# Kernel tuning notes

Hardware: AMD Instinct MI355X
Metric: run time of the kernel (lower is better)

Reference implementation:

```python
import jax, jax.numpy as jnp
import numpy as np

HID = 128; H = 8; D = HID // H; L = 2; IN = 128; OUT = 32
ND = 20000; NF = 50000; E = 400000
SQRT_D = float(np.sqrt(D))
LN_EPS = 1e-5


def setup_inputs() -> dict:
    key = jax.random.key(0)
    ks = jax.random.split(key, 16)
    s = 1.0 / np.sqrt(HID)
    n = lambda k, sh, sc=1.0: jax.random.normal(k, sh, jnp.float32) * sc
    return dict(
        x_device=n(ks[0], (ND, IN)),
        x_feature=n(ks[1], (NF, IN)),
        e_df_src=jax.random.randint(ks[2], (E,), 0, ND),
        e_df_dst=jax.random.randint(ks[3], (E,), 0, NF),
        e_fd_src=jax.random.randint(ks[4], (E,), 0, NF),
        e_fd_dst=jax.random.randint(ks[5], (E,), 0, ND),
        W_dev_in=n(ks[6], (IN, HID), s), b_dev_in=jnp.zeros((HID,), jnp.float32),
        W_feat_in=n(ks[7], (IN, HID), s), b_feat_in=jnp.zeros((HID,), jnp.float32),
        Wk=n(ks[8], (L, 2, HID, HID), s), bk=jnp.zeros((L, 2, HID), jnp.float32),
        Wq=n(ks[9], (L, 2, HID, HID), s), bq=jnp.zeros((L, 2, HID), jnp.float32),
        Wv=n(ks[10], (L, 2, HID, HID), s), bv=jnp.zeros((L, 2, HID), jnp.float32),
        a_rel=n(ks[11], (L, 2, H, D, D), 1.0 / np.sqrt(D)),
        m_rel=n(ks[12], (L, 2, H, D, D), 1.0 / np.sqrt(D)),
        p_rel=jnp.ones((L, 2, H), jnp.float32),
        Wa=n(ks[13], (L, 2, HID, HID), s), ba=jnp.zeros((L, 2, HID), jnp.float32),
        skip=jnp.ones((L, 2), jnp.float32),
        ln_g=jnp.ones((L, 2, HID), jnp.float32), ln_b=jnp.zeros((L, 2, HID), jnp.float32),
        W_out=n(ks[14], (HID, OUT), s), b_out=jnp.zeros((OUT,), jnp.float32),
    )


def _layer_norm(x, g, b):
    m = x.mean(-1, keepdims=True)
    v = ((x - m) ** 2).mean(-1, keepdims=True)
    return (x - m) * jax.lax.rsqrt(v + LN_EPS) * g + b


def _edge_agg(q_dst, k_src, v_src, a_r, m_r, p_r, src, dst, n_dst):
    # per-edge-type relation transforms of source k/v: [N_src,H,D]
    kt = jnp.einsum('nhd,hde->nhe', k_src, a_r)
    vt = jnp.einsum('nhd,hde->nhe', v_src, m_r)
    # per-edge attention logits [E,H], scaled by relation prior
    logit = (q_dst[dst] * kt[src]).sum(-1) * p_r / SQRT_D
    # segment softmax over incoming edges of each dst node (per edge type)
    mx = jax.ops.segment_max(logit, dst, num_segments=n_dst)
    ex = jnp.exp(logit - mx[dst])
    sm = jax.ops.segment_sum(ex, dst, num_segments=n_dst)
    alpha = ex / (sm[dst] + 1e-16)
    # attention-weighted message scatter-sum -> [n_dst,H,D]
    return jax.ops.segment_sum(vt[src] * alpha[..., None], dst, num_segments=n_dst)


def _forward(x_device, x_feature, W_dev_in, b_dev_in, W_feat_in, b_feat_in,
             Wk, bk, Wq, bq, Wv, bv, a_rel, m_rel, p_rel, Wa, ba, skip,
             ln_g, ln_b, W_out, b_out, e_df_src, e_df_dst, e_fd_src, e_fd_dst):
    x_d = jax.nn.relu(x_device @ W_dev_in + b_dev_in)
    x_f = jax.nn.relu(x_feature @ W_feat_in + b_feat_in)
    for l in range(L):
        xs = (x_d, x_f)  # node-type 0 = device, 1 = feature
        k = [(xs[t] @ Wk[l, t] + bk[l, t]).reshape(-1, H, D) for t in range(2)]
        q = [(xs[t] @ Wq[l, t] + bq[l, t]).reshape(-1, H, D) for t in range(2)]
        v = [(xs[t] @ Wv[l, t] + bv[l, t]).reshape(-1, H, D) for t in range(2)]
        # edge type 0: device -> feature ; edge type 1: feature -> device
        agg_f = _edge_agg(q[1], k[0], v[0], a_rel[l, 0], m_rel[l, 0], p_rel[l, 0],
                          e_df_src, e_df_dst, NF)
        agg_d = _edge_agg(q[0], k[1], v[1], a_rel[l, 1], m_rel[l, 1], p_rel[l, 1],
                          e_fd_src, e_fd_dst, ND)
        new = []
        for t, agg in ((0, agg_d), (1, agg_f)):
            o = jax.nn.gelu(agg.reshape(-1, HID), approximate=False) @ Wa[l, t] + ba[l, t]
            sk = jax.nn.sigmoid(skip[l, t])
            o = sk * o + (1.0 - sk) * xs[t]              # HGTConv skip
            new.append(_layer_norm(xs[t] + o, ln_g[l, t], ln_b[l, t]))  # wrapper residual+LN (dropout=identity in eval)
        x_d, x_f = new
    return x_d @ W_out + b_out


def reference(x_device, x_feature, e_df_src, e_df_dst, e_fd_src, e_fd_dst,
              W_dev_in, b_dev_in, W_feat_in, b_feat_in, Wk, bk, Wq, bq, Wv, bv,
              a_rel, m_rel, p_rel, Wa, ba, skip, ln_g, ln_b, W_out, b_out):
    return _forward(x_device, x_feature, W_dev_in, b_dev_in, W_feat_in, b_feat_in,
                    Wk, bk, Wq, bq, Wv, bv, a_rel, m_rel, p_rel, Wa, ba, skip,
                    ln_g, ln_b, W_out, b_out, e_df_src, e_df_dst, e_fd_src, e_fd_dst)
```

## Files before the change

kernel.cpp:

```cpp
#include <hip/hip_runtime.h>
#include <math.h>

#define ND 20000
#define NF 50000
#define NE 400000
#define NT (NF + ND)
#define NBKT 256
#define BKTW 274

typedef __attribute__((ext_vector_type(8))) short short8;
typedef __attribute__((ext_vector_type(4))) float f32x4;
typedef unsigned short us;

static __device__ __forceinline__ us f2bf(float f) {
    unsigned u = __builtin_bit_cast(unsigned, f);
    u += 0x7FFF + ((u >> 16) & 1);
    return (us)(u >> 16);
}
static __device__ __forceinline__ float bf2f(us h) {
    return __builtin_bit_cast(float, (unsigned)h << 16);
}
static __device__ __forceinline__ float bflo(unsigned u) {
    return __builtin_bit_cast(float, u << 16);
}
static __device__ __forceinline__ float bfhi(unsigned u) {
    return __builtin_bit_cast(float, u & 0xFFFF0000u);
}
static __device__ __forceinline__ float gelu_f(float x) {
    return 0.5f * x * (1.0f + erff(x * 0.70710678118654752f));
}

__global__ void k_hist_prep(const int* __restrict__ dA, const int* __restrict__ dB,
                            int* __restrict__ blockhist, int HB,
                            const float* __restrict__ W_dev_in, const float* __restrict__ W_feat_in,
                            const float* __restrict__ Wq, const float* __restrict__ Wk,
                            const float* __restrict__ Wv, const float* __restrict__ Wa,
                            const float* __restrict__ b_dev_in, const float* __restrict__ b_feat_in,
                            const float* __restrict__ bq, const float* __restrict__ bk,
                            const float* __restrict__ bv, const float* __restrict__ ba,
                            const float* __restrict__ a_rel, const float* __restrict__ m_rel,
                            const float* __restrict__ p_rel,
                            us* __restrict__ WT, float* __restrict__ B_all) {
    __shared__ int hist[NBKT];
    if ((int)blockIdx.x < HB) {
        hist[threadIdx.x] = 0;
        __syncthreads();
        int base_e = blockIdx.x * 4096;
        #pragma unroll
        for (int j = 0; j < 16; ++j) {
            int e = base_e + j * 256 + threadIdx.x;
            if (e < 2 * NE) {
                int g = (e < NE) ? dA[e] : (NF + dB[e - NE]);
                atomicAdd(&hist[g / BKTW], 1);
            }
        }
        __syncthreads();
        blockhist[blockIdx.x * NBKT + threadIdx.x] = hist[threadIdx.x];
        return;
    }
    int idx = (blockIdx.x - HB) * 256 + threadIdx.x;
    if (idx < 18 * 16384) {
        int k = idx & 127, c = (idx >> 7) & 127, id = idx >> 14;
        float val;
        if (id == 0) val = W_dev_in[k * 128 + c];
        else if (id == 1) val = W_feat_in[k * 128 + c];
        else if (id < 6) val = Wq[(id - 2) * 16384 + k * 128 + c];
        else if (id < 10) {
            int lt = id - 6, h = c >> 4, e = c & 15;
            const float* A = a_rel + (lt * 8 + h) * 256;
            const float* Ws = Wk + lt * 16384 + k * 128 + h * 16;
            float sm = 0.f;
            #pragma unroll
            for (int d = 0; d < 16; ++d) sm += Ws[d] * A[d * 16 + e];
            val = sm * p_rel[lt * 8 + h] * 0.25f;
        } else if (id < 14) {
            int lt = id - 10, h = c >> 4, e = c & 15;
            const float* A = m_rel + (lt * 8 + h) * 256;
            const float* Ws = Wv + lt * 16384 + k * 128 + h * 16;
            float sm = 0.f;
            #pragma unroll
            for (int d = 0; d < 16; ++d) sm += Ws[d] * A[d * 16 + e];
            val = sm;
        } else val = Wa[(id - 14) * 16384 + k * 128 + c];
        WT[(size_t)id * 16384 + (((c * 128 + k)) ^ ((c & 7) << 3))] = f2bf(val);
    } else {
        int j = idx - 18 * 16384;
        if (j >= 18 * 128) return;
        int c = j & 127, id = j >> 7;
        float v;
        if (id == 0) v = b_dev_in[c];
        else if (id == 1) v = b_feat_in[c];
        else if (id < 6) v = bq[(id - 2) * 128 + c];
        else if (id < 10) {
            int lt = id - 6, h = c >> 4, e = c & 15;
            const float* A = a_rel + (lt * 8 + h) * 256;
            const float* bs = bk + lt * 128 + h * 16;
            float sm = 0.f;
            #pragma unroll
            for (int d = 0; d < 16; ++d) sm += bs[d] * A[d * 16 + e];
            v = sm * p_rel[lt * 8 + h] * 0.25f;
        } else if (id < 14) {
            int lt = id - 10, h = c >> 4, e = c & 15;
            const float* A = m_rel + (lt * 8 + h) * 256;
            const float* bs = bv + lt * 128 + h * 16;
            float sm = 0.f;
            #pragma unroll
            for (int d = 0; d < 16; ++d) sm += bs[d] * A[d * 16 + e];
            v = sm;
        } else v = ba[(id - 14) * 128 + c];
        B_all[j] = v;
    }
}

__global__ void k_scanA(int* __restrict__ blockhist, int* __restrict__ totals, int HB) {
    __shared__ int sd[256];
    int b = blockIdx.x, t = threadIdx.x;
    int v = (t < HB) ? blockhist[t * NBKT + b] : 0;
    sd[t] = v; __syncthreads();
    for (int off = 1; off < 256; off <<= 1) {
        int add = (t >= off) ? sd[t - off] : 0;
        __syncthreads();
        sd[t] += add;
        __syncthreads();
    }
    if (t < HB) blockhist[t * NBKT + b] = sd[t] - v;
    if (t == 255) totals[b] = sd[255];
}

__global__ void k_scanB(const int* __restrict__ totals, int* __restrict__ base) {
    __shared__ int sd[256];
    int t = threadIdx.x;
    int v = totals[t];
    sd[t] = v; __syncthreads();
    for (int off = 1; off < 256; off <<= 1) {
        int add = (t >= off) ? sd[t - off] : 0;
        __syncthreads();
        sd[t] += add;
        __syncthreads();
    }
    base[t] = sd[t] - v;
    if (t == 255) base[256] = sd[255];
}

__global__ void k_scatter(const int* __restrict__ sA, const int* __restrict__ dA,
                          const int* __restrict__ sB, const int* __restrict__ dB,
                          const int* __restrict__ blockhist, const int* __restrict__ base,
                          uint2* __restrict__ pairs) {
    __shared__ int lcur[NBKT];
    int t = threadIdx.x;
    lcur[t] = base[t] + blockhist[blockIdx.x * NBKT + t];
    __syncthreads();
    int base_e = blockIdx.x * 4096;
    #pragma unroll
    for (int j = 0; j < 16; ++j) {
        int e = base_e + j * 256 + t;
        if (e < 2 * NE) {
            int src, g;
            if (e < NE) { src = sA[e]; g = dA[e]; }
            else        { src = sB[e - NE]; g = NF + dB[e - NE]; }
            int pos = atomicAdd(&lcur[g / BKTW], 1);
            pairs[pos] = make_uint2((unsigned)src, (unsigned)g);
        }
    }
}

__global__ void k_bucket_csr(const uint2* __restrict__ pairs, const int* __restrict__ base,
                             int* __restrict__ rs, int* __restrict__ esrc) {
    __shared__ int cnt[BKTW];
    __shared__ int excl[BKTW];
    int b = blockIdx.x, t = threadIdx.x;
    int start = base[b], end = base[b + 1];
    int g0 = b * BKTW;
    for (int i = t; i < BKTW; i += 256) cnt[i] = 0;
    __syncthreads();
    for (int i = start + t; i < end; i += 256)
        atomicAdd(&cnt[(int)pairs[i].y - g0], 1);
    __syncthreads();
    if (t < 64) {
        int lane = t;
        int vals[5]; int s = 0;
        #pragma unroll
        for (int j = 0; j < 5; ++j) {
            int i = lane * 5 + j;
            vals[j] = (i < BKTW) ? cnt[i] : 0;
            s += vals[j];
        }
        int incl = s;
        #pragma unroll
        for (int off = 1; off < 64; off <<= 1) {
            int n = __shfl_up(incl, off);
            if (lane >= off) incl += n;
        }
        int run = incl - s;
        #pragma unroll
        for (int j = 0; j < 5; ++j) {
            int i = lane * 5 + j;
            if (i < BKTW) excl[i] = run;
            run += vals[j];
        }
    }
    __syncthreads();
    int nloc = min(BKTW, NT - g0);
    for (int i = t; i < nloc; i += 256) rs[g0 + i] = start + excl[i];
    if (b == NBKT - 1 && t == 0) rs[NT] = base[NBKT];
    __syncthreads();
    for (int i = start + t; i < end; i += 256) {
        uint2 p = pairs[i];
        int pos = start + atomicAdd(&excl[(int)p.y - g0], 1);
        esrc[pos] = (int)p.x;
    }
}

template<int MODE, int AF32, int RELU>
__global__ __launch_bounds__(256) void mfma_gemm2(
    const void* __restrict__ X0, const void* __restrict__ X1,
    const us* __restrict__ WT0, const float* __restrict__ Ball,
    us* __restrict__ Y0, us* __restrict__ Y1,
    int N0, int N1, int GB0, int widbase,
    us* __restrict__ K0, us* __restrict__ K1,
    const float* __restrict__ skipv, const float* __restrict__ lng,
    const float* __restrict__ lnb) {
    __shared__ us Wlds[16384];
    const int type = (blockIdx.x >= (unsigned)GB0) ? 1 : 0;
    const int bx = blockIdx.x - (type ? GB0 : 0);
    const int N = type ? N1 : N0;
    const void* Xv = type ? X1 : X0;
    const int NP = (MODE == 1) ? 3 : 1;

    const int lane = threadIdx.x & 63;
    const int wave = threadIdx.x >> 6;
    const int row_base = bx * 128 + wave * 32;
    const int l15 = lane & 15, lg = lane >> 4;
    const int kbase = lg * 8;

    const char* gsrc0 = (const char*)(WT0 + (size_t)(widbase + type) * 16384)
                        + wave * 8192 + lane * 16;
    {
        char* ldst = (char*)Wlds + wave * 8192;
        #pragma unroll
        for (int i = 0; i < 8; ++i) {
            __builtin_amdgcn_global_load_lds(
                (const __attribute__((address_space(1))) void*)(gsrc0 + i * 1024),
                (__attribute__((address_space(3))) void*)(ldst + i * 1024),
                16, 0, 0);
        }
    }

    short8 a[2][4];
    #pragma unroll
    for (int mf = 0; mf < 2; ++mf) {
        int r = row_base + mf * 16 + l15;
        r = r < N ? r : N - 1;
        if (AF32) {
            const float* Xf = (const float*)Xv + (size_t)r * 128;
            #pragma unroll
            for (int kf = 0; kf < 4; ++kf) {
                float4 lo = *(const float4*)(Xf + kf * 32 + kbase);
                float4 hi = *(const float4*)(Xf + kf * 32 + kbase + 4);
                short8 t;
                t[0] = (short)f2bf(lo.x); t[1] = (short)f2bf(lo.y);
                t[2] = (short)f2bf(lo.z); t[3] = (short)f2bf(lo.w);
                t[4] = (short)f2bf(hi.x); t[5] = (short)f2bf(hi.y);
                t[6] = (short)f2bf(hi.z); t[7] = (short)f2bf(hi.w);
                a[mf][kf] = t;
            }
        } else {
            const us* Xb = (const us*)Xv + (size_t)r * 128;
            #pragma unroll
            for (int kf = 0; kf < 4; ++kf)
                a[mf][kf] = *(const short8*)(Xb + kf * 32 + kbase);
        }
    }

    __syncthreads();

    const unsigned swz = (unsigned)((l15 & 7) << 4);

    for (int p = 0; p < NP; ++p) {
        const int wid = widbase + type + 4 * p;
        const float* bias = Ball + wid * 128;

        f32x4 acc[2][8];
        #pragma unroll
        for (int mf = 0; mf < 2; ++mf)
            #pragma unroll
            for (int cf = 0; cf < 8; ++cf) acc[mf][cf] = (f32x4){0.f, 0.f, 0.f, 0.f};

        #pragma unroll
        for (int cf = 0; cf < 8; ++cf) {
            const unsigned rowbyte = (unsigned)((cf * 16 + l15) * 256 + kbase * 2);
            #pragma unroll
            for (int kf = 0; kf < 4; ++kf) {
                short8 b = *(const short8*)((const char*)Wlds + ((rowbyte + kf * 64) ^ swz));
                acc[0][cf] = __builtin_amdgcn_mfma_f32_16x16x32_bf16(a[0][kf], b, acc[0][cf], 0, 0, 0);
                acc[1][cf] = __builtin_amdgcn_mfma_f32_16x16x32_bf16(a[1][kf], b, acc[1][cf], 0, 0, 0);
            }
        }

        if (MODE == 1 && p + 1 < NP) {
            __syncthreads();
            const char* gsrc = (const char*)(WT0 + (size_t)(widbase + type + 4 * (p + 1)) * 16384)
                               + wave * 8192 + lane * 16;
            char* ldst = (char*)Wlds + wave * 8192;
            #pragma unroll
            for (int i = 0; i < 8; ++i) {
                __builtin_amdgcn_global_load_lds(
                    (const __attribute__((address_space(1))) void*)(gsrc + i * 1024),
                    (__attribute__((address_space(3))) void*)(ldst + i * 1024),
                    16, 0, 0);
            }
        }

        float bval[8];
        #pragma unroll
        for (int cf = 0; cf < 8; ++cf) bval[cf] = bias[cf * 16 + l15];

        if (MODE == 2) {
            const int lt = widbase - 14 + type;
            float sk = 1.f / (1.f + __expf(-skipv[lt]));
            float gv[8], bv2[8];
            #pragma unroll
            for (int cf = 0; cf < 8; ++cf) {
                gv[cf]  = lng[(size_t)lt * 128 + cf * 16 + l15];
                bv2[cf] = lnb[(size_t)lt * 128 + cf * 16 + l15];
            }
            us* xw = type ? K1 : K0;
            #pragma unroll
            for (int mf = 0; mf < 2; ++mf)
                #pragma unroll
                for (int r = 0; r < 4; ++r) {
                    int grow = row_base + mf * 16 + lg * 4 + r;
                    if (grow >= N) continue;
                    float t[8];
                    float sum = 0.f;
                    #pragma unroll
                    for (int cf = 0; cf < 8; ++cf) {
                        float o = acc[mf][cf][r] + bval[cf];
                        float x = bf2f(xw[(size_t)grow * 128 + cf * 16 + l15]);
                        t[cf] = (2.f - sk) * x + sk * o;
                        sum += t[cf];
                    }
                    sum += __shfl_xor(sum, 1); sum += __shfl_xor(sum, 2);
                    sum += __shfl_xor(sum, 4); sum += __shfl_xor(sum, 8);
                    float mean = sum * (1.0f / 128.0f);
                    float vs = 0.f;
                    #pragma unroll
                    for (int cf = 0; cf < 8; ++cf) { t[cf] -= mean; vs += t[cf] * t[cf]; }
                    vs += __shfl_xor(vs, 1); vs += __shfl_xor(vs, 2);
                    vs += __shfl_xor(vs, 4); vs += __shfl_xor(vs, 8);
                    float inv = rsqrtf(vs * (1.0f / 128.0f) + 1e-5f);
                    #pragma unroll
                    for (int cf = 0; cf < 8; ++cf)
                        xw[(size_t)grow * 128 + cf * 16 + l15] = f2bf(t[cf] * inv * gv[cf] + bv2[cf]);
                }
        } else {
            #pragma unroll
            for (int mf = 0; mf < 2; ++mf)
                #pragma unroll
                for (int r = 0; r < 4; ++r) {
                    int grow = row_base + mf * 16 + lg * 4 + r;
                    if (grow >= N) continue;
                    #pragma unroll
                    for (int cf = 0; cf < 8; ++cf) {
                        float v = acc[mf][cf][r] + bval[cf];
                        if (RELU) v = fmaxf(v, 0.f);
                        us val = f2bf(v);
                        int col = cf * 16 + l15;
                        if (MODE == 0 || p == 0) {
                            (type ? Y1 : Y0)[(size_t)grow * 128 + col] = val;
                        } else {
                            (type ? K1 : K0)[(size_t)grow * 256 + (p - 1) * 128 + col] = val;
                        }
                    }
                }
        }

        if (MODE == 1 && p + 1 < NP) __syncthreads();
    }
}

__global__ __launch_bounds__(256) void gemm_out_k(
    const us* __restrict__ X, const float* __restrict__ W,
    const float* __restrict__ bias, float* __restrict__ Y, int N) {
    __shared__ float Ws[128 * 32];
    __shared__ float Xs[8][128];
    const int tid = threadIdx.x;
    const int row0 = blockIdx.x * 8;
    #pragma unroll
    for (int it = 0; it < 16; ++it) Ws[it * 256 + tid] = W[it * 256 + tid];
    #pragma unroll
    for (int it = 0; it < 2; ++it) {
        int idx = it * 256 + tid;
        int rr = idx >> 6, kp = idx & 63;
        int gr = row0 + rr;
        unsigned u = (gr < N) ? *(const unsigned*)(X + (size_t)gr * 128 + kp * 2) : 0u;
        Xs[rr][kp * 2]     = bflo(u);
        Xs[rr][kp * 2 + 1] = bfhi(u);
    }
    __syncthreads();
    const int rr = tid >> 5, c = tid & 31;
    float acc = bias[c];
    #pragma unroll 8
    for (int k = 0; k < 128; ++k)
        acc = fmaf(Xs[rr][k], Ws[k * 32 + c], acc);
    int gr = row0 + rr;
    if (gr < N) Y[(size_t)gr * 32 + c] = acc;
}

#define EDGE_STEP(kc, vc, pidx)                                        \
    {                                                                  \
        float part = qv[0] * bflo(kc.x);                               \
        part = fmaf(qv[1], bfhi(kc.x), part);                          \
        part = fmaf(qv[2], bflo(kc.y), part);                          \
        part = fmaf(qv[3], bfhi(kc.y), part);                          \
        part = fmaf(qv[4], bflo(kc.z), part);                          \
        part = fmaf(qv[5], bfhi(kc.z), part);                          \
        part = fmaf(qv[6], bflo(kc.w), part);                          \
        part = fmaf(qv[7], bfhi(kc.w), part);                          \
        part += __shfl_xor(part, 1);                                   \
        float w = ((pidx) < p1) ? __expf(part) : 0.f;                  \
        s += w;                                                        \
        a[0] = fmaf(w, bflo(vc.x), a[0]);                              \
        a[1] = fmaf(w, bfhi(vc.x), a[1]);                              \
        a[2] = fmaf(w, bflo(vc.y), a[2]);                              \
        a[3] = fmaf(w, bfhi(vc.y), a[3]);                              \
        a[4] = fmaf(w, bflo(vc.z), a[4]);                              \
        a[5] = fmaf(w, bfhi(vc.z), a[5]);                              \
        a[6] = fmaf(w, bflo(vc.w), a[6]);                              \
        a[7] = fmaf(w, bfhi(vc.w), a[7]);                              \
    }

__global__ __launch_bounds__(256) void edge_agg5(
    const us* __restrict__ qf, const us* __restrict__ qd,
    const us* __restrict__ kvf, const us* __restrict__ kvd,
    const int* __restrict__ rs, const int* __restrict__ esrc,
    us* __restrict__ aggf, us* __restrict__ aggd) {
    int g = (blockIdx.x * 256 + threadIdx.x) >> 4;
    int li = threadIdx.x & 15;
    if (g >= NT) return;
    const us *q, *kv; us* agg; int dst;
    if (g < NF) { dst = g;      q = qf; kv = kvd; agg = aggf; }
    else        { dst = g - NF; q = qd; kv = kvf; agg = aggd; }

    uint4 qb = *(const uint4*)(q + (size_t)dst * 128 + li * 8);
    float qv[8];
    qv[0] = bflo(qb.x); qv[1] = bfhi(qb.x);
    qv[2] = bflo(qb.y); qv[3] = bfhi(qb.y);
    qv[4] = bflo(qb.z); qv[5] = bfhi(qb.z);
    qv[6] = bflo(qb.w); qv[7] = bfhi(qb.w);

    const int p0 = rs[g], p1 = rs[g + 1];
    float s = 0.f;
    float a[8];
    #pragma unroll
    for (int j = 0; j < 8; ++j) a[j] = 0.f;

    const size_t loff = (size_t)li * 8;
    uint4 kA0, vA0, kA1, vA1, kB0, vB0, kB1, vB1;
    int sN0, sN1, sN2, sN3;

    if (p0 < p1) {
        const int last = p1 - 1;
        int i0 = p0, i1 = min(p0 + 1, last), i2 = min(p0 + 2, last), i3 = min(p0 + 3, last);
        int s0 = esrc[i0], s1 = esrc[i1], s2 = esrc[i2], s3 = esrc[i3];
        kA0 = *(const uint4*)(kv + (size_t)s0 * 256 + loff);
        vA0 = *(const uint4*)(kv + (size_t)s0 * 256 + 128 + loff);
        kA1 = *(const uint4*)(kv + (size_t)s1 * 256 + loff);
        vA1 = *(const uint4*)(kv + (size_t)s1 * 256 + 128 + loff);
        kB0 = *(const uint4*)(kv + (size_t)s2 * 256 + loff);
        vB0 = *(const uint4*)(kv + (size_t)s2 * 256 + 128 + loff);
        kB1 = *(const uint4*)(kv + (size_t)s3 * 256 + loff);
        vB1 = *(const uint4*)(kv + (size_t)s3 * 256 + 128 + loff);
        sN0 = esrc[min(p0 + 4, last)];
        sN1 = esrc[min(p0 + 5, last)];
        sN2 = esrc[min(p0 + 6, last)];
        sN3 = esrc[min(p0 + 7, last)];

        for (int p = p0; p < p1; p += 4) {
            const int lastc = last;
            EDGE_STEP(kA0, vA0, p);
            EDGE_STEP(kA1, vA1, p + 1);
            kA0 = *(const uint4*)(kv + (size_t)sN0 * 256 + loff);
            vA0 = *(const uint4*)(kv + (size_t)sN0 * 256 + 128 + loff);
            kA1 = *(const uint4*)(kv + (size_t)sN1 * 256 + loff);
            vA1 = *(const uint4*)(kv + (size_t)sN1 * 256 + 128 + loff);
            sN0 = esrc[min(p + 8, lastc)];
            sN1 = esrc[min(p + 9, lastc)];
            EDGE_STEP(kB0, vB0, p + 2);
            EDGE_STEP(kB1, vB1, p + 3);
            kB0 = *(const uint4*)(kv + (size_t)sN2 * 256 + loff);
            vB0 = *(const uint4*)(kv + (size_t)sN2 * 256 + 128 + loff);
            kB1 = *(const uint4*)(kv + (size_t)sN3 * 256 + loff);
            vB1 = *(const uint4*)(kv + (size_t)sN3 * 256 + 128 + loff);
            sN2 = esrc[min(p + 10, lastc)];
            sN3 = esrc[min(p + 11, lastc)];
        }
    }

    float r = 1.0f / (s + 1e-16f);
    unsigned o[4];
    #pragma unroll
    for (int j = 0; j < 4; ++j) {
        us lo = f2bf(gelu_f(a[2 * j] * r));
        us hi = f2bf(gelu_f(a[2 * j + 1] * r));
        o[j] = (unsigned)lo | ((unsigned)hi << 16);
    }
    *(uint4*)(agg + (size_t)dst * 128 + li * 8) = make_uint4(o[0], o[1], o[2], o[3]);
}

extern "C" void kernel_launch(void* const* d_in, const int* in_sizes, int n_in,
                              void* d_out, int out_size, void* d_ws, size_t ws_size,
                              hipStream_t stream) {
    const float* x_device = (const float*)d_in[0];
    const float* x_feature = (const float*)d_in[1];
    const int* e_df_src = (const int*)d_in[2];
    const int* e_df_dst = (const int*)d_in[3];
    const int* e_fd_src = (const int*)d_in[4];
    const int* e_fd_dst = (const int*)d_in[5];
    const float* W_dev_in = (const float*)d_in[6];
    const float* b_dev_in = (const float*)d_in[7];
    const float* W_feat_in = (const float*)d_in[8];
    const float* b_feat_in = (const float*)d_in[9];
    const float* Wk = (const float*)d_in[10];
    const float* bk = (const float*)d_in[11];
    const float* Wq = (const float*)d_in[12];
    const float* bq = (const float*)d_in[13];
    const float* Wv = (const float*)d_in[14];
    const float* bv = (const float*)d_in[15];
    const float* a_rel = (const float*)d_in[16];
    const float* m_rel = (const float*)d_in[17];
    const float* p_rel = (const float*)d_in[18];
    const float* Wa = (const float*)d_in[19];
    const float* ba = (const float*)d_in[20];
    const float* skip = (const float*)d_in[21];
    const float* ln_g = (const float*)d_in[22];
    const float* ln_b = (const float*)d_in[23];
    const float* W_out = (const float*)d_in[24];
    const float* b_out = (const float*)d_in[25];

    char* ws = (char*)d_ws;
    size_t off = 0;
    auto alloc = [&](size_t bytes) -> void* {
        void* p = ws + off;
        off = (off + bytes + 255) & ~(size_t)255;
        return p;
    };
    us* xd     = (us*)alloc((size_t)ND * 128 * 2);
    us* xf     = (us*)alloc((size_t)NF * 128 * 2);
    us* q_d    = (us*)alloc((size_t)ND * 128 * 2);
    us* q_f    = (us*)alloc((size_t)NF * 128 * 2);
    us* kv_d   = (us*)alloc((size_t)ND * 256 * 2);
    us* kv_f   = (us*)alloc((size_t)NF * 256 * 2);
    us* agg_d  = (us*)alloc((size_t)ND * 128 * 2);
    us* agg_f  = (us*)alloc((size_t)NF * 128 * 2);
    us* WT     = (us*)alloc((size_t)18 * 16384 * 2);
    float* B_all = (float*)alloc(18 * 128 * 4);
    int* rs     = (int*)alloc((size_t)(NT + 1) * 4);
    int* esrc   = (int*)alloc((size_t)(2 * NE + 8) * 4);
    uint2* pairs = (uint2*)alloc((size_t)2 * NE * 8);
    int* blockhist = (int*)alloc((size_t)200 * NBKT * 4);
    int* totals = (int*)alloc(NBKT * 4);
    int* base   = (int*)alloc((NBKT + 1) * 4);

    const int HB = (2 * NE + 4095) / 4096;
    const int PB = (18 * 16384 + 18 * 128 + 255) / 256;

    k_hist_prep<<<HB + PB, 256, 0, stream>>>(
        e_df_dst, e_fd_dst, blockhist, HB,
        W_dev_in, W_feat_in, Wq, Wk, Wv, Wa,
        b_dev_in, b_feat_in, bq, bk, bv, ba,
        a_rel, m_rel, p_rel, WT, B_all);
    k_scanA<<<NBKT, 256, 0, stream>>>(blockhist, totals, HB);
    k_scanB<<<1, 256, 0, stream>>>(totals, base);
    k_scatter<<<HB, 256, 0, stream>>>(e_df_src, e_df_dst, e_fd_src, e_fd_dst,
                                      blockhist, base, pairs);
    k_bucket_csr<<<NBKT, 256, 0, stream>>>(pairs, base, rs, esrc);

    const int GBD = (ND + 127) / 128, GBF = (NF + 127) / 128;

    mfma_gemm2<0, 1, 1><<<GBD + GBF, 256, 0, stream>>>(
        x_device, x_feature, WT, B_all, xd, xf, ND, NF, GBD, 0,
        nullptr, nullptr, nullptr, nullptr, nullptr);

    for (int l = 0; l < 2; ++l) {
        mfma_gemm2<1, 0, 0><<<GBD + GBF, 256, 0, stream>>>(
            xd, xf, WT, B_all, q_d, q_f, ND, NF, GBD, 2 + l * 2,
            kv_d, kv_f, nullptr, nullptr, nullptr);

        edge_agg5<<<((NT * 16) + 255) / 256, 256, 0, stream>>>(
            q_f, q_d, kv_f, kv_d, rs, esrc, agg_f, agg_d);

        mfma_gemm2<2, 0, 0><<<GBD + GBF, 256, 0, stream>>>(
            agg_d, agg_f, WT, B_all, nullptr, nullptr, ND, NF, GBD, 14 + l * 2,
            xd, xf, skip, ln_g, ln_b);
    }

    gemm_out_k<<<(ND + 7) / 8, 256, 0, stream>>>(xd, W_out, b_out, (float*)d_out, ND);
}
```

Baseline: 267.7 us.

## Store V in FP8 and split K/V buffers; fold bucket scan into consumers

The QKV GEMM now writes K as a separate bf16 array and V as a separate FP8 (e4m3) array, and edge aggregation reads 8 bytes of V per lane instead of 16, decoding with the hardware pk_f32_fp8 conversion. This cuts the gather traffic in the memory-bound edge kernel. Separately, the single-block k_scanB launch is removed and its 256-wide prefix scan is recomputed redundantly inside k_scatter and k_bucket_csr. FP8 values lose precision, which risks tolerance failures, and the redundant scans add a little work per block.

```diff
diff --git a/kernel.cpp b/kernel.cpp
--- a/kernel.cpp
+++ b/kernel.cpp
@@ -10,7 +10,9 @@
 
 typedef __attribute__((ext_vector_type(8))) short short8;
 typedef __attribute__((ext_vector_type(4))) float f32x4;
+typedef __attribute__((ext_vector_type(2))) float f32x2;
 typedef unsigned short us;
+typedef unsigned char u8;
 
 static __device__ __forceinline__ us f2bf(float f) {
     unsigned u = __builtin_bit_cast(unsigned, f);
@@ -28,6 +30,22 @@
 }
 static __device__ __forceinline__ float gelu_f(float x) {
     return 0.5f * x * (1.0f + erff(x * 0.70710678118654752f));
+}
+
+static __device__ __forceinline__ u8 f2fp8(float f) {
+    unsigned u = __builtin_bit_cast(unsigned, f);
+    unsigned s = (u >> 24) & 0x80u;
+    unsigned a = u & 0x7FFFFFFFu;
+    if (a >= 0x43E00000u) return (u8)(s | 0x7Eu);
+    if (a < 0x3C800000u) {
+        float af = __builtin_bit_cast(float, a);
+        unsigned q = (unsigned)(af * 512.0f + 0.5f);
+        return (u8)(s | q);
+    }
+    unsigned r = a + 0x7FFFFu + ((a >> 20) & 1u);
+    unsigned e8 = (r >> 23) - 120u;
+    unsigned m3 = (r >> 20) & 7u;
+    return (u8)(s | (e8 << 3) | m3);
 }
 
 __global__ void k_hist_prep(const int* __restrict__ dA, const int* __restrict__ dB,
@@ -127,28 +145,22 @@
     if (t == 255) totals[b] = sd[255];
 }
 
-__global__ void k_scanB(const int* __restrict__ totals, int* __restrict__ base) {
-    __shared__ int sd[256];
-    int t = threadIdx.x;
-    int v = totals[t];
-    sd[t] = v; __syncthreads();
-    for (int off = 1; off < 256; off <<= 1) {
-        int add = (t >= off) ? sd[t - off] : 0;
-        __syncthreads();
-        sd[t] += add;
-        __syncthreads();
-    }
-    base[t] = sd[t] - v;
-    if (t == 255) base[256] = sd[255];
-}
-
 __global__ void k_scatter(const int* __restrict__ sA, const int* __restrict__ dA,
                           const int* __restrict__ sB, const int* __restrict__ dB,
-                          const int* __restrict__ blockhist, const int* __restrict__ base,
+                          const int* __restrict__ blockhist, const int* __restrict__ totals,
                           uint2* __restrict__ pairs) {
     __shared__ int lcur[NBKT];
+    __shared__ int sdb[NBKT];
     int t = threadIdx.x;
-    lcur[t] = base[t] + blockhist[blockIdx.x * NBKT + t];
+    int tv = totals[t];
+    sdb[t] = tv; __syncthreads();
+    for (int off = 1; off < 256; off <<= 1) {
+        int add = (t >= off) ? sdb[t - off] : 0;
+        __syncthreads();
+        sdb[t] += add;
+        __syncthreads();
+    }
+    lcur[t] = (sdb[t] - tv) + blockhist[blockIdx.x * NBKT + t];
     __syncthreads();
     int base_e = blockIdx.x * 4096;
     #pragma unroll
@@ -164,12 +176,24 @@
     }
 }
 
-__global__ void k_bucket_csr(const uint2* __restrict__ pairs, const int* __restrict__ base,
+__global__ void k_bucket_csr(const uint2* __restrict__ pairs, const int* __restrict__ totals,
                              int* __restrict__ rs, int* __restrict__ esrc) {
     __shared__ int cnt[BKTW];
     __shared__ int excl[BKTW];
+    __shared__ int sdb[NBKT];
+    __shared__ int sde[NBKT];
     int b = blockIdx.x, t = threadIdx.x;
-    int start = base[b], end = base[b + 1];
+    int tv = totals[t];
+    sdb[t] = tv; __syncthreads();
+    for (int off = 1; off < 256; off <<= 1) {
+        int add = (t >= off) ? sdb[t - off] : 0;
+        __syncthreads();
+        sdb[t] += add;
+        __syncthreads();
+    }
+    sde[t] = sdb[t] - tv;
+    __syncthreads();
+    int start = sde[b], end = sdb[b];
     int g0 = b * BKTW;
     for (int i = t; i < BKTW; i += 256) cnt[i] = 0;
     __syncthreads();
@@ -202,7 +226,7 @@
     __syncthreads();
     int nloc = min(BKTW, NT - g0);
     for (int i = t; i < nloc; i += 256) rs[g0 + i] = start + excl[i];
-    if (b == NBKT - 1 && t == 0) rs[NT] = base[NBKT];
+    if (b == NBKT - 1 && t == 0) rs[NT] = sdb[255];
     __syncthreads();
     for (int i = start + t; i < end; i += 256) {
         uint2 p = pairs[i];
@@ -218,6 +242,7 @@
     us* __restrict__ Y0, us* __restrict__ Y1,
     int N0, int N1, int GB0, int widbase,
     us* __restrict__ K0, us* __restrict__ K1,
+    u8* __restrict__ V0, u8* __restrict__ V1,
     const float* __restrict__ skipv, const float* __restrict__ lng,
     const float* __restrict__ lnb) {
     __shared__ us Wlds[16384];
@@ -233,14 +258,14 @@
     const int l15 = lane & 15, lg = lane >> 4;
     const int kbase = lg * 8;
 
-    const char* gsrc0 = (const char*)(WT0 + (size_t)(widbase + type) * 16384)
-                        + wave * 8192 + lane * 16;
     {
+        const char* gsrc = (const char*)(WT0 + (size_t)(widbase + type) * 16384)
+                           + wave * 8192 + lane * 16;
         char* ldst = (char*)Wlds + wave * 8192;
         #pragma unroll
         for (int i = 0; i < 8; ++i) {
             __builtin_amdgcn_global_load_lds(
-                (const __attribute__((address_space(1))) void*)(gsrc0 + i * 1024),
+                (const __attribute__((address_space(1))) void*)(gsrc + i * 1024),
                 (__attribute__((address_space(3))) void*)(ldst + i * 1024),
                 16, 0, 0);
         }
@@ -364,12 +389,13 @@
                     for (int cf = 0; cf < 8; ++cf) {
                         float v = acc[mf][cf][r] + bval[cf];
                         if (RELU) v = fmaxf(v, 0.f);
-                        us val = f2bf(v);
                         int col = cf * 16 + l15;
                         if (MODE == 0 || p == 0) {
-                            (type ? Y1 : Y0)[(size_t)grow * 128 + col] = val;
+                            (type ? Y1 : Y0)[(size_t)grow * 128 + col] = f2bf(v);
+                        } else if (p == 1) {
+                            (type ? K1 : K0)[(size_t)grow * 128 + col] = f2bf(v);
                         } else {
-                            (type ? K1 : K0)[(size_t)grow * 256 + (p - 1) * 128 + col] = val;
+                            (type ? V1 : V0)[(size_t)grow * 128 + col] = f2fp8(v);
                         }
                     }
                 }
@@ -420,27 +446,32 @@
         part += __shfl_xor(part, 1);                                   \
         float w = ((pidx) < p1) ? __expf(part) : 0.f;                  \
         s += w;                                                        \
-        a[0] = fmaf(w, bflo(vc.x), a[0]);                              \
-        a[1] = fmaf(w, bfhi(vc.x), a[1]);                              \
-        a[2] = fmaf(w, bflo(vc.y), a[2]);                              \
-        a[3] = fmaf(w, bfhi(vc.y), a[3]);                              \
-        a[4] = fmaf(w, bflo(vc.z), a[4]);                              \
-        a[5] = fmaf(w, bfhi(vc.z), a[5]);                              \
-        a[6] = fmaf(w, bflo(vc.w), a[6]);                              \
-        a[7] = fmaf(w, bfhi(vc.w), a[7]);                              \
-    }
-
-__global__ __launch_bounds__(256) void edge_agg5(
+        f32x2 v01 = __builtin_amdgcn_cvt_pk_f32_fp8((int)vc.x, false); \
+        f32x2 v23 = __builtin_amdgcn_cvt_pk_f32_fp8((int)vc.x, true);  \
+        f32x2 v45 = __builtin_amdgcn_cvt_pk_f32_fp8((int)vc.y, false); \
+        f32x2 v67 = __builtin_amdgcn_cvt_pk_f32_fp8((int)vc.y, true);  \
+        a[0] = fmaf(w, v01.x, a[0]);                                   \
+        a[1] = fmaf(w, v01.y, a[1]);                                   \
+        a[2] = fmaf(w, v23.x, a[2]);                                   \
+        a[3] = fmaf(w, v23.y, a[3]);                                   \
+        a[4] = fmaf(w, v45.x, a[4]);                                   \
+        a[5] = fmaf(w, v45.y, a[5]);                                   \
+        a[6] = fmaf(w, v67.x, a[6]);                                   \
+        a[7] = fmaf(w, v67.y, a[7]);                                   \
+    }
+
+__global__ __launch_bounds__(256) void edge_agg6(
     const us* __restrict__ qf, const us* __restrict__ qd,
-    const us* __restrict__ kvf, const us* __restrict__ kvd,
+    const us* __restrict__ ktf, const us* __restrict__ ktd,
+    const u8* __restrict__ v8f, const u8* __restrict__ v8d,
     const int* __restrict__ rs, const int* __restrict__ esrc,
     us* __restrict__ aggf, us* __restrict__ aggd) {
     int g = (blockIdx.x * 256 + threadIdx.x) >> 4;
     int li = threadIdx.x & 15;
     if (g >= NT) return;
-    const us *q, *kv; us* agg; int dst;
-    if (g < NF) { dst = g;      q = qf; kv = kvd; agg = aggf; }
-    else        { dst = g - NF; q = qd; kv = kvf; agg = aggd; }
+    const us *q, *kt; const u8* v8; us* agg; int dst;
+    if (g < NF) { dst = g;      q = qf; kt = ktd; v8 = v8d; agg = aggf; }
+    else        { dst = g - NF; q = qd; kt = ktf; v8 = v8f; agg = aggd; }
 
     uint4 qb = *(const uint4*)(q + (size_t)dst * 128 + li * 8);
     float qv[8];
@@ -456,21 +487,22 @@
     for (int j = 0; j < 8; ++j) a[j] = 0.f;
 
     const size_t loff = (size_t)li * 8;
-    uint4 kA0, vA0, kA1, vA1, kB0, vB0, kB1, vB1;
+    uint4 kA0, kA1, kB0, kB1;
+    uint2 vA0, vA1, vB0, vB1;
     int sN0, sN1, sN2, sN3;
 
     if (p0 < p1) {
         const int last = p1 - 1;
-        int i0 = p0, i1 = min(p0 + 1, last), i2 = min(p0 + 2, last), i3 = min(p0 + 3, last);
-        int s0 = esrc[i0], s1 = esrc[i1], s2 = esrc[i2], s3 = esrc[i3];
-        kA0 = *(const uint4*)(kv + (size_t)s0 * 256 + loff);
-        vA0 = *(const uint4*)(kv + (size_t)s0 * 256 + 128 + loff);
-        kA1 = *(const uint4*)(kv + (size_t)s1 * 256 + loff);
-        vA1 = *(const uint4*)(kv + (size_t)s1 * 256 + 128 + loff);
-        kB0 = *(const uint4*)(kv + (size_t)s2 * 256 + loff);
-        vB0 = *(const uint4*)(kv + (size_t)s2 * 256 + 128 + loff);
-        kB1 = *(const uint4*)(kv + (size_t)s3 * 256 + loff);
-        vB1 = *(const uint4*)(kv + (size_t)s3 * 256 + 128 + loff);
+        int s0 = esrc[p0], s1 = esrc[min(p0 + 1, last)];
+        int s2 = esrc[min(p0 + 2, last)], s3 = esrc[min(p0 + 3, last)];
+        kA0 = *(const uint4*)(kt + (size_t)s0 * 128 + loff);
+        vA0 = *(const uint2*)(v8 + (size_t)s0 * 128 + loff);
+        kA1 = *(const uint4*)(kt + (size_t)s1 * 128 + loff);
+        vA1 = *(const uint2*)(v8 + (size_t)s1 * 128 + loff);
+        kB0 = *(const uint4*)(kt + (size_t)s2 * 128 + loff);
+        vB0 = *(const uint2*)(v8 + (size_t)s2 * 128 + loff);
+        kB1 = *(const uint4*)(kt + (size_t)s3 * 128 + loff);
+        vB1 = *(const uint2*)(v8 + (size_t)s3 * 128 + loff);
         sN0 = esrc[min(p0 + 4, last)];
         sN1 = esrc[min(p0 + 5, last)];
         sN2 = esrc[min(p0 + 6, last)];
@@ -480,18 +512,18 @@
             const int lastc = last;
             EDGE_STEP(kA0, vA0, p);
             EDGE_STEP(kA1, vA1, p + 1);
-            kA0 = *(const uint4*)(kv + (size_t)sN0 * 256 + loff);
-            vA0 = *(const uint4*)(kv + (size_t)sN0 * 256 + 128 + loff);
-            kA1 = *(const uint4*)(kv + (size_t)sN1 * 256 + loff);
-            vA1 = *(const uint4*)(kv + (size_t)sN1 * 256 + 128 + loff);
+            kA0 = *(const uint4*)(kt + (size_t)sN0 * 128 + loff);
+            vA0 = *(const uint2*)(v8 + (size_t)sN0 * 128 + loff);
+            kA1 = *(const uint4*)(kt + (size_t)sN1 * 128 + loff);
+            vA1 = *(const uint2*)(v8 + (size_t)sN1 * 128 + loff);
             sN0 = esrc[min(p + 8, lastc)];
             sN1 = esrc[min(p + 9, lastc)];
             EDGE_STEP(kB0, vB0, p + 2);
             EDGE_STEP(kB1, vB1, p + 3);
-            kB0 = *(const uint4*)(kv + (size_t)sN2 * 256 + loff);
-            vB0 = *(const uint4*)(kv + (size_t)sN2 * 256 + 128 + loff);
-            kB1 = *(const uint4*)(kv + (size_t)sN3 * 256 + loff);
-            vB1 = *(const uint4*)(kv + (size_t)sN3 * 256 + 128 + loff);
+            kB0 = *(const uint4*)(kt + (size_t)sN2 * 128 + loff);
+            vB0 = *(const uint2*)(v8 + (size_t)sN2 * 128 + loff);
+            kB1 = *(const uint4*)(kt + (size_t)sN3 * 128 + loff);
+            vB1 = *(const uint2*)(v8 + (size_t)sN3 * 128 + loff);
             sN2 = esrc[min(p + 10, lastc)];
             sN3 = esrc[min(p + 11, lastc)];
         }
@@ -549,8 +581,10 @@
     us* xf     = (us*)alloc((size_t)NF * 128 * 2);
     us* q_d    = (us*)alloc((size_t)ND * 128 * 2);
     us* q_f    = (us*)alloc((size_t)NF * 128 * 2);
-    us* kv_d   = (us*)alloc((size_t)ND * 256 * 2);
-    us* kv_f   = (us*)alloc((size_t)NF * 256 * 2);
+    us* kt_d   = (us*)alloc((size_t)ND * 128 * 2);
+    us* kt_f   = (us*)alloc((size_t)NF * 128 * 2);
+    u8* v8_d   = (u8*)alloc((size_t)ND * 128);
+    u8* v8_f   = (u8*)alloc((size_t)NF * 128);
     us* agg_d  = (us*)alloc((size_t)ND * 128 * 2);
     us* agg_f  = (us*)alloc((size_t)NF * 128 * 2);
     us* WT     = (us*)alloc((size_t)18 * 16384 * 2);
@@ -560,7 +594,6 @@
     uint2* pairs = (uint2*)alloc((size_t)2 * NE * 8);
     int* blockhist = (int*)alloc((size_t)200 * NBKT * 4);
     int* totals = (int*)alloc(NBKT * 4);
-    int* base   = (int*)alloc((NBKT + 1) * 4);
 
     const int HB = (2 * NE + 4095) / 4096;
     const int PB = (18 * 16384 + 18 * 128 + 255) / 256;
@@ -571,28 +604,27 @@
         b_dev_in, b_feat_in, bq, bk, bv, ba,
         a_rel, m_rel, p_rel, WT, B_all);
     k_scanA<<<NBKT, 256, 0, stream>>>(blockhist, totals, HB);
-    k_scanB<<<1, 256, 0, stream>>>(totals, base);
     k_scatter<<<HB, 256, 0, stream>>>(e_df_src, e_df_dst, e_fd_src, e_fd_dst,
-                                      blockhist, base, pairs);
-    k_bucket_csr<<<NBKT, 256, 0, stream>>>(pairs, base, rs, esrc);
+                                      blockhist, totals, pairs);
+    k_bucket_csr<<<NBKT, 256, 0, stream>>>(pairs, totals, rs, esrc);
 
     const int GBD = (ND + 127) / 128, GBF = (NF + 127) / 128;
 
     mfma_gemm2<0, 1, 1><<<GBD + GBF, 256, 0, stream>>>(
         x_device, x_feature, WT, B_all, xd, xf, ND, NF, GBD, 0,
-        nullptr, nullptr, nullptr, nullptr, nullptr);
+        nullptr, nullptr, nullptr, nullptr, nullptr, nullptr, nullptr);
 
     for (int l = 0; l < 2; ++l) {
         mfma_gemm2<1, 0, 0><<<GBD + GBF, 256, 0, stream>>>(
             xd, xf, WT, B_all, q_d, q_f, ND, NF, GBD, 2 + l * 2,
-            kv_d, kv_f, nullptr, nullptr, nullptr);
-
-        edge_agg5<<<((NT * 16) + 255) / 256, 256, 0, stream>>>(
-            q_f, q_d, kv_f, kv_d, rs, esrc, agg_f, agg_d);
+            kt_d, kt_f, v8_d, v8_f, nullptr, nullptr, nullptr);
+
+        edge_agg6<<<((NT * 16) + 255) / 256, 256, 0, stream>>>(
+            q_f, q_d, kt_f, kt_d, v8_f, v8_d, rs, esrc, agg_f, agg_d);
 
         mfma_gemm2<2, 0, 0><<<GBD + GBF, 256, 0, stream>>>(
             agg_d, agg_f, WT, B_all, nullptr, nullptr, ND, NF, GBD, 14 + l * 2,
-            xd, xf, skip, ln_g, ln_b);
+            xd, xf, nullptr, nullptr, skip, ln_g, ln_b);
     }
 
     gemm_out_k<<<(ND + 7) / 8, 256, 0, stream>>>(xd, W_out, b_out, (float*)d_out, ND);
```

New measurement: 257.1 us, median of 2. -4.0%, faster.
